# Optimization experiments

Measured on AMD Instinct MI355X. Metric: run time of the kernel, lower is better.

## Reference

```python
import jax, jax.numpy as jnp
import numpy as np
import math

EPS = 1e-8
DIM, HEADS, K = 256, 8, 16
HD = DIM // HEADS
B, N, PDIM = 4, 4096, 3


def _layernorm(x, w, b, eps=1e-5):
    m = jnp.mean(x, axis=-1, keepdims=True)
    v = jnp.mean((x - m) ** 2, axis=-1, keepdims=True)
    return (x - m) * jax.lax.rsqrt(v + eps) * w + b


def setup_inputs() -> dict:
    key = jax.random.key(0)
    ks = jax.random.split(key, 16)
    s = 0.02
    d = {
        'x': jax.random.normal(ks[0], (B, N, DIM), jnp.float32),
        'positions': jax.random.uniform(ks[1], (B, N, PDIM), jnp.float32) * 0.5,  # inside unit ball
        'c': jnp.ones((1,), jnp.float32),
        'time_emb': jax.random.normal(ks[2], (B, DIM), jnp.float32),
        'Wq': jax.random.normal(ks[3], (DIM, DIM), jnp.float32) * s,
        'bq': jnp.zeros((DIM,), jnp.float32),
        'Wk': jax.random.normal(ks[4], (DIM, DIM), jnp.float32) * s,
        'bk': jnp.zeros((DIM,), jnp.float32),
        'Wv': jax.random.normal(ks[5], (DIM, DIM), jnp.float32) * s,
        'bv': jnp.zeros((DIM,), jnp.float32),
        'Wo': jax.random.normal(ks[6], (DIM, DIM), jnp.float32) * s,
        'bo': jnp.zeros((DIM,), jnp.float32),
        'W1': jax.random.normal(ks[7], (DIM, 4 * DIM), jnp.float32) * s,
        'b1': jnp.zeros((4 * DIM,), jnp.float32),
        'W2': jax.random.normal(ks[8], (4 * DIM, DIM), jnp.float32) * s,
        'b2': jnp.zeros((DIM,), jnp.float32),
        'ln1_w': jnp.ones((DIM,), jnp.float32),
        'ln1_b': jnp.zeros((DIM,), jnp.float32),
        'ln2_w': jnp.ones((DIM,), jnp.float32),
        'ln2_b': jnp.zeros((DIM,), jnp.float32),
        'log_tau': jnp.zeros((), jnp.float32),
    }
    return d


def _poincare_dist_matrix(pos, c):
    # pos: [B,N,P], c: scalar > 0. Returns [B,N,N] with d[b,i,j] = dist(pos[b,j], pos[b,i])
    sq = jnp.sum(pos ** 2, axis=-1)                      # [B,N]
    diff2 = (sq[:, :, None] + sq[:, None, :]
             - 2.0 * jnp.einsum('bip,bjp->bij', pos, pos))
    diff2 = jnp.maximum(diff2, 0.0)
    num = 2.0 * c * diff2
    den = (1.0 - c * sq[:, :, None]) * (1.0 - c * sq[:, None, :])
    arg = jnp.maximum(1.0 + num / (den + EPS), 1.0)
    return jnp.arccosh(arg) / jnp.sqrt(c)


def reference(x, positions, c, time_emb, Wq, bq, Wk, bk, Wv, bv, Wo, bo,
              W1, b1, W2, b2, ln1_w, ln1_b, ln2_w, ln2_b, log_tau):
    c_s = jnp.squeeze(c)
    x_res = x
    h = _layernorm(x, ln1_w, ln1_b) + time_emb[:, None, :]

    q = (h @ Wq + bq).reshape(B, N, HEADS, HD).transpose(0, 2, 1, 3)  # [B,H,N,hd]
    k = (h @ Wk + bk).reshape(B, N, HEADS, HD).transpose(0, 2, 1, 3)
    v = (h @ Wv + bv).reshape(B, N, HEADS, HD).transpose(0, 2, 1, 3)

    # pairwise hyperbolic distances + kNN (no_grad in original)
    dist = jax.lax.stop_gradient(_poincare_dist_matrix(positions, c_s))  # [B,N,N]
    neg_vals, idx = jax.lax.top_k(-dist, K)          # smallest-K distances
    attn_dists = -neg_vals                            # [B,N,K]

    # gather neighbor keys/values: out[b,h,n,j,d] = k[b,h,idx[b,n,j],d]
    idx_flat = idx.reshape(B, 1, N * K, 1)            # broadcast over heads, hd
    k_g = jnp.take_along_axis(k, idx_flat, axis=2).reshape(B, HEADS, N, K, HD)
    v_g = jnp.take_along_axis(v, idx_flat, axis=2).reshape(B, HEADS, N, K, HD)

    feat = jnp.einsum('bhnd,bhnkd->bhnk', q, k_g) / math.sqrt(HD)
    tau = jnp.exp(log_tau) + EPS
    scores = feat - attn_dists[:, None, :, :] / tau
    probs = jax.nn.softmax(scores, axis=-1)
    attn = jnp.einsum('bhnk,bhnkd->bhnd', probs, v_g)
    attn = attn.transpose(0, 2, 1, 3).reshape(B, N, DIM)

    x2 = x_res + attn @ Wo + bo
    ff = jax.nn.gelu(_layernorm(x2, ln2_w, ln2_b) @ W1 + b1, approximate=False) @ W2 + b2
    return x2 + ff
```

## Files before the change

### kernel.cpp

```cpp
#include <hip/hip_runtime.h>
#include <math.h>

namespace {

constexpr int kBatch = 4;
constexpr int kN = 4096;
constexpr int kDim = 256;
constexpr int kHeads = 8;
constexpr int kK = 16;
constexpr float kEps = 1e-8f;

using u16 = unsigned short;
typedef __attribute__((ext_vector_type(8))) short short8;
typedef __attribute__((ext_vector_type(8))) u16 u16x8;
typedef __attribute__((ext_vector_type(4))) float f32x4;

__device__ __forceinline__ float b2f(u16 u) {
  union { unsigned int i; float f; } x; x.i = ((unsigned int)u) << 16; return x.f;
}
__device__ __forceinline__ u16 f2b(float f) {
  union { float f; unsigned int i; } x; x.f = f;
  unsigned int r = x.i + 0x7fffu + ((x.i >> 16) & 1u);
  return (u16)(r >> 16);
}
__device__ __forceinline__ float gelu_exact(float x) {
  return 0.5f * x * (1.0f + erff(x * 0.70710678118654752f));
}
__device__ __forceinline__ void load_lds16(const u16* g, u16* l) {
  __builtin_amdgcn_global_load_lds(
      (const __attribute__((address_space(1))) unsigned int*)g,
      (__attribute__((address_space(3))) unsigned int*)l, 16, 0, 0);
}

template<bool ADD_TEMB>
__device__ __forceinline__ void ln_body(
    const float* __restrict__ x, const float* __restrict__ w,
    const float* __restrict__ bb, const float* __restrict__ temb,
    u16* __restrict__ out, int gt) {
  int row = gt >> 6;
  int lane = gt & 63;
  const float4* xr = (const float4*)(x + (size_t)row * kDim);
  float4 v = xr[lane];
  float s = v.x + v.y + v.z + v.w;
  #pragma unroll
  for (int off = 32; off; off >>= 1) s += __shfl_xor(s, off);
  float mean = s * (1.0f / kDim);
  float dx = v.x - mean, dy = v.y - mean, dz = v.z - mean, dw = v.w - mean;
  float ss = dx * dx + dy * dy + dz * dz + dw * dw;
  #pragma unroll
  for (int off = 32; off; off >>= 1) ss += __shfl_xor(ss, off);
  float rstd = rsqrtf(ss * (1.0f / kDim) + 1e-5f);
  float4 wv = ((const float4*)w)[lane];
  float4 bv = ((const float4*)bb)[lane];
  float ox = dx * rstd * wv.x + bv.x;
  float oy = dy * rstd * wv.y + bv.y;
  float oz = dz * rstd * wv.z + bv.z;
  float ow = dw * rstd * wv.w + bv.w;
  if (ADD_TEMB) {
    int bi = row >> 12;
    float4 t = ((const float4*)(temb + (size_t)bi * kDim))[lane];
    ox += t.x; oy += t.y; oz += t.z; ow += t.w;
  }
  ushort4 ob;
  ob.x = f2b(ox); ob.y = f2b(oy); ob.z = f2b(oz); ob.w = f2b(ow);
  ((ushort4*)(out + (size_t)row * kDim))[lane] = ob;
}

__global__ __launch_bounds__(1024, 2) void front_kernel(
    const float* __restrict__ pos, const float* __restrict__ cptr,
    int* __restrict__ idx_out, float* __restrict__ dist_out,
    const float* __restrict__ x, const float* __restrict__ ln1w,
    const float* __restrict__ ln1b, const float* __restrict__ temb,
    u16* __restrict__ h_out,
    const float* __restrict__ Wq, const float* __restrict__ Wk,
    const float* __restrict__ Wv, const float* __restrict__ Wo,
    const float* __restrict__ W1, const float* __restrict__ W2,
    u16* __restrict__ Tq, u16* __restrict__ Tk,
    u16* __restrict__ Tv, u16* __restrict__ To,
    u16* __restrict__ T1, u16* __restrict__ T2) {
  __shared__ float4 ps[kN];
  int tid = threadIdx.x;
  int bx = blockIdx.x;

  if (bx >= 1024) {
    if (bx < 1216) {
      int sub = tid >> 8, stid = tid & 255;
      int task = (bx - 1024) * 4 + sub;
      float* tt = (float*)ps + sub * 1056;
      int seg = task >> 8, e = task & 255;
      const float* W; u16* T; int Kin, Nin, kt, nt;
      if (seg == 0) {
        int which = e >> 6, tl = e & 63;
        W = which == 0 ? Wq : which == 1 ? Wk : which == 2 ? Wv : Wo;
        T = which == 0 ? Tq : which == 1 ? Tk : which == 2 ? Tv : To;
        Kin = 256; Nin = 256; kt = tl >> 3; nt = tl & 7;
      } else if (seg == 1) {
        W = W1; T = T1; Kin = 256; Nin = 1024; kt = e >> 5; nt = e & 31;
      } else {
        W = W2; T = T2; Kin = 1024; Nin = 256; kt = e >> 3; nt = e & 7;
      }
      int tx = stid & 31, ty = stid >> 5;
      #pragma unroll
      for (int rr = 0; rr < 4; ++rr) {
        int r = rr * 8 + ty;
        tt[r * 33 + tx] = W[(size_t)(kt * 32 + r) * Nin + nt * 32 + tx];
      }
      __syncthreads();
      #pragma unroll
      for (int rr = 0; rr < 4; ++rr) {
        int r = rr * 8 + ty;
        T[(size_t)(nt * 32 + r) * Kin + kt * 32 + tx] = f2b(tt[tx * 33 + r]);
      }
    } else {
      ln_body<true>(x, ln1w, ln1b, temb, h_out, (bx - 1216) * 1024 + tid);
    }
    return;
  }

  int wave = tid >> 6, ln = tid & 63;
  int row = bx * 16 + wave;
  int b = row >> 12;
  float c = cptr[0];
  const float* pb = pos + (size_t)b * kN * 3;
  for (int j = tid; j < kN; j += 1024) {
    float px = pb[j * 3 + 0], py = pb[j * 3 + 1], pz = pb[j * 3 + 2];
    ps[j] = make_float4(px, py, pz, c * (px * px + py * py + pz * pz));
  }
  __syncthreads();

  int i = row & (kN - 1);
  float4 pi = ps[i];
  float wi = pi.w, oi = 1.0f - wi;
  float sx = 2.0f * c * pi.x, sy = 2.0f * c * pi.y, sz = 2.0f * c * pi.z;

  auto numden = [&](int j, float& num, float& den) {
    float4 pj = ps[j];
    float tt = wi + pj.w;
    tt = fmaf(-sx, pj.x, tt);
    tt = fmaf(-sy, pj.y, tt);
    tt = fmaf(-sz, pj.z, tt);
    num = fmaxf(tt, 0.0f);
    den = fmaf(-oi, pj.w, oi);
  };
  auto packkey = [&](float num, float den, int j) -> unsigned {
    float r = num * __builtin_amdgcn_rcpf(den);
    union { float f; unsigned u; } cv; cv.f = r;
    return (cv.u & 0xFFFFF000u) | (unsigned)j;
  };
  auto inflate = [&](unsigned T) -> float {
    union { unsigned u; float f; } tv; tv.u = T & 0xFFFFF000u;
    return fmaf(tv.f, 0.001f, tv.f);
  };

  float n0, d0;
  numden(ln, n0, d0);
  unsigned lpk = packkey(n0, d0, ln);
  #pragma unroll
  for (int kk = 2; kk <= 64; kk <<= 1) {
    #pragma unroll
    for (int jj = kk >> 1; jj >= 1; jj >>= 1) {
      unsigned ov = (unsigned)__shfl_xor((int)lpk, jj);
      bool keepMin = (((ln & kk) == 0) == ((ln & jj) == 0));
      bool less = ov < lpk;
      if (keepMin ? less : !less) lpk = ov;
    }
  }
  float Tf = inflate((unsigned)__builtin_amdgcn_readlane((int)lpk, 15));

  auto processGroup = [&](float num, float den, int base) {
    unsigned long long m = __ballot(num < Tf * den);
    if (m) {
      unsigned cpk = packkey(num, den, base + ln);
      do {
        int src = __ffsll(m) - 1;
        m &= m - 1;
        unsigned npk = (unsigned)__builtin_amdgcn_readlane((int)cpk, src);
        unsigned pv = (unsigned)__builtin_amdgcn_update_dpp(
            0, (int)lpk, 0x111 , 0xF, 0xF, false);
        bool gt = lpk > npk;
        bool take = gt && ((ln == 0) || (pv <= npk));
        lpk = take ? npk : (gt ? pv : lpk);
      } while (m);
      Tf = inflate((unsigned)__builtin_amdgcn_readlane((int)lpk, 15));
    }
  };

  int t = 1;
  for (; t + 3 < 64; t += 4) {
    float a0, b0, a1, b1, a2, b2, a3, b3;
    numden(ln + (t + 0) * 64, a0, b0);
    numden(ln + (t + 1) * 64, a1, b1);
    numden(ln + (t + 2) * 64, a2, b2);
    numden(ln + (t + 3) * 64, a3, b3);
    processGroup(a0, b0, (t + 0) * 64);
    processGroup(a1, b1, (t + 1) * 64);
    processGroup(a2, b2, (t + 2) * 64);
    processGroup(a3, b3, (t + 3) * 64);
  }
  for (; t < 64; ++t) {
    float a0, b0;
    numden(ln + t * 64, a0, b0);
    processGroup(a0, b0, t * 64);
  }

  if (ln < kK) {
    int j = (int)(lpk & 0xFFFu);
    float4 pj = ps[j];
    float tt = wi + pj.w;
    tt = fmaf(-sx, pj.x, tt);
    tt = fmaf(-sy, pj.y, tt);
    tt = fmaf(-sz, pj.z, tt);
    float num = 2.0f * fmaxf(tt, 0.0f);
    float den = fmaf(-oi, pj.w, oi) + kEps;
    float arg = fmaxf(1.0f + num / den, 1.0f);
    float rs = 1.0f / sqrtf(c);
    idx_out[(size_t)row * kK + ln] = j;
    dist_out[(size_t)row * kK + ln] = acoshf(arg) * rs;
  }
}

template<int EPI, int BN>
__device__ __forceinline__ void gemm_body(
    const u16* __restrict__ A, const u16* __restrict__ Bt,
    const float* __restrict__ bias, const float* __restrict__ R,
    float* __restrict__ Cf, u16* __restrict__ Cbf,
    int N, int K, int bx, int by) {
  constexpr int NI = BN / 32;
  constexpr int BK = 64;
  __shared__ u16 Al[128 * BK];
  __shared__ u16 Bl[BN * BK];
  int tid = threadIdx.x;
  int wv = tid >> 6, ln = tid & 63;
  int wr = wv >> 1, wc = wv & 1;
  int lhi = ln >> 4, llo = ln & 15;
  int bm = bx * 128, bn = by * BN;

  f32x4 zero = {0.f, 0.f, 0.f, 0.f};
  f32x4 acc[4][NI];
  #pragma unroll
  for (int mi = 0; mi < 4; ++mi)
    #pragma unroll
    for (int ni = 0; ni < NI; ++ni) acc[mi][ni] = zero;

  for (int k0 = 0; k0 < K; k0 += BK) {
    if (k0) __syncthreads();
    #pragma unroll
    for (int i = 0; i < 128 * BK / (8 * 256); ++i) {
      int f = i * 256 + tid;
      int r = f >> 3, o = f & 7;
      load_lds16(A + (size_t)(bm + r) * K + k0 + ((o ^ (r & 7)) << 3),
                 &Al[(i * 256 + wv * 64) * 8]);
    }
    #pragma unroll
    for (int i = 0; i < BN * BK / (8 * 256); ++i) {
      int f = i * 256 + tid;
      int r = f >> 3, o = f & 7;
      load_lds16(Bt + (size_t)(bn + r) * K + k0 + ((o ^ (r & 7)) << 3),
                 &Bl[(i * 256 + wv * 64) * 8]);
    }
    __syncthreads();
    #pragma unroll
    for (int ks = 0; ks < BK; ks += 32) {
      short8 af[4], bf[NI];
      #pragma unroll
      for (int mi = 0; mi < 4; ++mi) {
        int row = wr * 64 + mi * 16 + llo;
        int oct = ((ks >> 3) + lhi) ^ (llo & 7);
        af[mi] = *(const short8*)&Al[row * BK + oct * 8];
      }
      #pragma unroll
      for (int ni = 0; ni < NI; ++ni) {
        int row = wc * (BN / 2) + ni * 16 + llo;
        int oct = ((ks >> 3) + lhi) ^ (llo & 7);
        bf[ni] = *(const short8*)&Bl[row * BK + oct * 8];
      }
      #pragma unroll
      for (int mi = 0; mi < 4; ++mi)
        #pragma unroll
        for (int ni = 0; ni < NI; ++ni)
          acc[mi][ni] = __builtin_amdgcn_mfma_f32_16x16x32_bf16(
              af[mi], bf[ni], acc[mi][ni], 0, 0, 0);
    }
  }

  #pragma unroll
  for (int mi = 0; mi < 4; ++mi) {
    #pragma unroll
    for (int r = 0; r < 4; ++r) {
      int row = bm + wr * 64 + mi * 16 + lhi * 4 + r;
      #pragma unroll
      for (int ni = 0; ni < NI; ++ni) {
        int col = bn + wc * (BN / 2) + ni * 16 + llo;
        float val = acc[mi][ni][r] + bias[col];
        if (EPI == 1) {
          val += R[(size_t)row * N + col];
          Cf[(size_t)row * N + col] = val;
        } else {
          if (EPI == 2) val = gelu_exact(val);
          Cbf[(size_t)row * N + col] = f2b(val);
        }
      }
    }
  }
}

template<int EPI, int BN, int NY>
__global__ __launch_bounds__(256) void gemm_swz_kernel(
    const u16* __restrict__ A, const u16* __restrict__ Bt,
    const float* __restrict__ bias, const float* __restrict__ R,
    float* __restrict__ Cf, u16* __restrict__ Cbf, int N, int K) {
  int cpx = gridDim.x >> 3;
  int orig = blockIdx.x;
  int swz = (orig & 7) * cpx + (orig >> 3);
  int bx = swz / NY, by = swz % NY;
  gemm_body<EPI, BN>(A, Bt, bias, R, Cf, Cbf, N, K, bx, by);
}

__global__ __launch_bounds__(256) void qkv_kernel(
    const u16* __restrict__ A,
    const u16* __restrict__ Bq, const u16* __restrict__ Bk, const u16* __restrict__ Bv,
    const float* __restrict__ bq, const float* __restrict__ bk, const float* __restrict__ bv,
    u16* __restrict__ q, u16* __restrict__ k, u16* __restrict__ v) {
  int cpx = gridDim.x >> 3;
  int orig = blockIdx.x;
  int swz = (orig & 7) * cpx + (orig >> 3);
  int bx = swz / 6, y = swz % 6;
  int sel = y >> 1;
  const u16* Bt = sel == 0 ? Bq : sel == 1 ? Bk : Bv;
  const float* bias = sel == 0 ? bq : sel == 1 ? bk : bv;
  u16* C = sel == 0 ? q : sel == 1 ? k : v;
  gemm_body<0, 128>(A, Bt, bias, nullptr, nullptr, C, 256, 256, bx, y & 1);
}

__global__ __launch_bounds__(512) void wo_ln_kernel(
    const u16* __restrict__ A, const u16* __restrict__ Bt,
    const float* __restrict__ bo, const float* __restrict__ xres,
    const float* __restrict__ ln2w, const float* __restrict__ ln2b,
    float* __restrict__ x2, u16* __restrict__ tln) {
  __shared__ u16 Al[64 * 64];
  __shared__ u16 Bl[256 * 64];
  __shared__ float red[4][64][2];
  int tid = threadIdx.x;
  int wv = tid >> 6, ln = tid & 63;
  int wr = wv >> 2, wc = wv & 3;
  int lhi = ln >> 4, llo = ln & 15;
  int bm = blockIdx.x * 64;

  f32x4 zero = {0.f, 0.f, 0.f, 0.f};
  f32x4 acc[2][4];
  #pragma unroll
  for (int mi = 0; mi < 2; ++mi)
    #pragma unroll
    for (int ni = 0; ni < 4; ++ni) acc[mi][ni] = zero;

  for (int k0 = 0; k0 < 256; k0 += 64) {
    if (k0) __syncthreads();
    {
      int f = tid, r = f >> 3, o = f & 7;
      load_lds16(A + (size_t)(bm + r) * 256 + k0 + ((o ^ (r & 7)) << 3),
                 &Al[(wv * 64) * 8]);
    }
    #pragma unroll
    for (int i = 0; i < 4; ++i) {
      int f = i * 512 + tid, r = f >> 3, o = f & 7;
      load_lds16(Bt + (size_t)r * 256 + k0 + ((o ^ (r & 7)) << 3),
                 &Bl[((i * 8 + wv) * 64) * 8]);
    }
    __syncthreads();
    #pragma unroll
    for (int ks = 0; ks < 64; ks += 32) {
      short8 af[2], bf[4];
      #pragma unroll
      for (int mi = 0; mi < 2; ++mi) {
        int row = wr * 32 + mi * 16 + llo;
        int oct = ((ks >> 3) + lhi) ^ (llo & 7);
        af[mi] = *(const short8*)&Al[row * 64 + oct * 8];
      }
      #pragma unroll
      for (int ni = 0; ni < 4; ++ni) {
        int brow = wc * 64 + ni * 16 + llo;
        int oct = ((ks >> 3) + lhi) ^ (llo & 7);
        bf[ni] = *(const short8*)&Bl[brow * 64 + oct * 8];
      }
      #pragma unroll
      for (int mi = 0; mi < 2; ++mi)
        #pragma unroll
        for (int ni = 0; ni < 4; ++ni)
          acc[mi][ni] = __builtin_amdgcn_mfma_f32_16x16x32_bf16(
              af[mi], bf[ni], acc[mi][ni], 0, 0, 0);
    }
  }

  float psum[2][4], psq[2][4];
  #pragma unroll
  for (int mi = 0; mi < 2; ++mi) {
    #pragma unroll
    for (int r = 0; r < 4; ++r) {
      int row = bm + wr * 32 + mi * 16 + lhi * 4 + r;
      float s = 0.0f, q = 0.0f;
      #pragma unroll
      for (int ni = 0; ni < 4; ++ni) {
        int col = wc * 64 + ni * 16 + llo;
        float v = acc[mi][ni][r] + bo[col] + xres[(size_t)row * 256 + col];
        acc[mi][ni][r] = v;
        s += v;
        q = fmaf(v, v, q);
      }
      #pragma unroll
      for (int off = 1; off < 16; off <<= 1) {
        s += __shfl_xor(s, off);
        q += __shfl_xor(q, off);
      }
      psum[mi][r] = s; psq[mi][r] = q;
    }
  }
  if (llo == 0) {
    #pragma unroll
    for (int mi = 0; mi < 2; ++mi)
      #pragma unroll
      for (int r = 0; r < 4; ++r) {
        int rl = wr * 32 + mi * 16 + lhi * 4 + r;
        red[wc][rl][0] = psum[mi][r];
        red[wc][rl][1] = psq[mi][r];
      }
  }
  __syncthreads();
  constexpr float rn = 1.0f / 256.0f;
  #pragma unroll
  for (int mi = 0; mi < 2; ++mi) {
    #pragma unroll
    for (int r = 0; r < 4; ++r) {
      int rl = wr * 32 + mi * 16 + lhi * 4 + r;
      int row = bm + rl;
      float S = red[0][rl][0] + red[1][rl][0] + red[2][rl][0] + red[3][rl][0];
      float Q = red[0][rl][1] + red[1][rl][1] + red[2][rl][1] + red[3][rl][1];
      float mean = S * rn;
      float var = Q * rn - mean * mean;
      float rstd = rsqrtf(var + 1e-5f);
      #pragma unroll
      for (int ni = 0; ni < 4; ++ni) {
        int col = wc * 64 + ni * 16 + llo;
        float v = acc[mi][ni][r];
        x2[(size_t)row * 256 + col] = v;
        tln[(size_t)row * 256 + col] =
            f2b((v - mean) * rstd * ln2w[col] + ln2b[col]);
      }
    }
  }
}

__global__ __launch_bounds__(256) void attn_kernel(
    const u16* __restrict__ q, const u16* __restrict__ k,
    const u16* __restrict__ v, const int* __restrict__ nidx,
    const float* __restrict__ ndist, const float* __restrict__ log_tau,
    u16* __restrict__ out) {
  int t = blockIdx.x * 256 + threadIdx.x;
  int h = t & (kHeads - 1);
  int row = t >> 3;
  int b = row >> 12;
  float rtau = 1.0f / (expf(log_tau[0]) + kEps);
  const u16x8* qr = (const u16x8*)(q + (size_t)row * kDim + h * 32);
  float qf[32];
  #pragma unroll
  for (int cch = 0; cch < 4; ++cch) {
    u16x8 u = qr[cch];
    #pragma unroll
    for (int e = 0; e < 8; ++e) qf[cch * 8 + e] = b2f(u[e]);
  }

  int njs[kK];
  float sc[kK];
  const int* ir = nidx + (size_t)row * kK;
  const float* dr = ndist + (size_t)row * kK;
  float smax = -1e30f;
  #pragma unroll
  for (int j = 0; j < kK; ++j) {
    int nj = ir[j];
    njs[j] = nj;
    const u16x8* kr = (const u16x8*)(k + ((size_t)b * kN + nj) * kDim + h * 32);
    float dot = 0.0f;
    #pragma unroll
    for (int cch = 0; cch < 4; ++cch) {
      u16x8 u = kr[cch];
      #pragma unroll
      for (int e = 0; e < 8; ++e) dot = fmaf(qf[cch * 8 + e], b2f(u[e]), dot);
    }
    float s = dot * 0.17677669529663687f - dr[j] * rtau;
    sc[j] = s;
    smax = fmaxf(smax, s);
  }
  float sum = 0.0f;
  #pragma unroll
  for (int j = 0; j < kK; ++j) { sc[j] = expf(sc[j] - smax); sum += sc[j]; }
  float rsum = 1.0f / sum;
  float o[32];
  #pragma unroll
  for (int d = 0; d < 32; ++d) o[d] = 0.0f;
  #pragma unroll
  for (int j = 0; j < kK; ++j) {
    float p = sc[j] * rsum;
    const u16x8* vr = (const u16x8*)(v + ((size_t)b * kN + njs[j]) * kDim + h * 32);
    #pragma unroll
    for (int cch = 0; cch < 4; ++cch) {
      u16x8 u = vr[cch];
      #pragma unroll
      for (int e = 0; e < 8; ++e) o[cch * 8 + e] = fmaf(p, b2f(u[e]), o[cch * 8 + e]);
    }
  }
  u16x8* orow = (u16x8*)(out + (size_t)row * kDim + h * 32);
  #pragma unroll
  for (int cch = 0; cch < 4; ++cch) {
    u16x8 po;
    #pragma unroll
    for (int e = 0; e < 8; ++e) po[e] = f2b(o[cch * 8 + e]);
    orow[cch] = po;
  }
}

}

extern "C" void kernel_launch(void* const* d_in, const int* in_sizes, int n_in,
                              void* d_out, int out_size, void* d_ws, size_t ws_size,
                              hipStream_t stream) {
  const float* x    = (const float*)d_in[0];
  const float* pos  = (const float*)d_in[1];
  const float* c    = (const float*)d_in[2];
  const float* temb = (const float*)d_in[3];
  const float* Wq   = (const float*)d_in[4];
  const float* bq   = (const float*)d_in[5];
  const float* Wk   = (const float*)d_in[6];
  const float* bk   = (const float*)d_in[7];
  const float* Wv   = (const float*)d_in[8];
  const float* bv   = (const float*)d_in[9];
  const float* Wo   = (const float*)d_in[10];
  const float* bo   = (const float*)d_in[11];
  const float* W1   = (const float*)d_in[12];
  const float* b1   = (const float*)d_in[13];
  const float* W2   = (const float*)d_in[14];
  const float* b2   = (const float*)d_in[15];
  const float* ln1w = (const float*)d_in[16];
  const float* ln1b = (const float*)d_in[17];
  const float* ln2w = (const float*)d_in[18];
  const float* ln2b = (const float*)d_in[19];
  const float* ltau = (const float*)d_in[20];

  const size_t MB = 1ull << 20;
  char* w = (char*)d_ws;
  u16*   h_bf  = (u16*)(w + 0 * MB);
  u16*   qb    = (u16*)(w + 8 * MB);
  u16*   kb    = (u16*)(w + 16 * MB);
  u16*   vb    = (u16*)(w + 24 * MB);
  u16*   attnb = (u16*)(w + 32 * MB);
  float* x2    = (float*)(w + 40 * MB);
  u16*   g_bf  = (u16*)(w + 56 * MB);
  u16*   wq_t  = (u16*)(w + 88 * MB);
  u16*   wk_t  = wq_t + 65536;
  u16*   wv_t  = wq_t + 2 * 65536;
  u16*   wo_t  = wq_t + 3 * 65536;
  u16*   w1_t  = (u16*)(w + 89 * MB);
  u16*   w2_t  = (u16*)(w + 89 * MB + 512 * 1024);
  int*   kidx  = (int*)(w + 90 * MB);
  float* kdst  = (float*)(w + 91 * MB);
  u16*   tln   = h_bf;

  hipLaunchKernelGGL(front_kernel, dim3(2240), dim3(1024), 0, stream,
                     pos, c, kidx, kdst,
                     x, ln1w, ln1b, temb, h_bf,
                     Wq, Wk, Wv, Wo, W1, W2, wq_t, wk_t, wv_t, wo_t, w1_t, w2_t);
  hipLaunchKernelGGL(qkv_kernel, dim3(768), dim3(256), 0, stream,
                     h_bf, wq_t, wk_t, wv_t, bq, bk, bv, qb, kb, vb);
  hipLaunchKernelGGL(attn_kernel, dim3(512), dim3(256), 0, stream,
                     qb, kb, vb, kidx, kdst, ltau, attnb);
  hipLaunchKernelGGL(wo_ln_kernel, dim3(256), dim3(512), 0, stream,
                     attnb, wo_t, bo, x, ln2w, ln2b, x2, tln);
  hipLaunchKernelGGL((gemm_swz_kernel<2, 128, 8>), dim3(1024), dim3(256), 0, stream,
                     tln, w1_t, b1, nullptr, (float*)nullptr, g_bf, 1024, 256);
  hipLaunchKernelGGL((gemm_swz_kernel<1, 64, 4>), dim3(512), dim3(256), 0, stream,
                     g_bf, w2_t, b2, x2, (float*)d_out, (u16*)nullptr, 256, 1024);
}
```

Measured before the change: 163.2 us.

## Fuse kNN attention into Wo+LayerNorm kernel and simplify kNN threshold test

Removes the standalone attention kernel. Each block of the Wo/LayerNorm kernel now computes the gathered-neighbor attention for its 64 rows and writes the result straight into a swizzled LDS tile, which drops one kernel launch and the global round trip of the attention output. Separately, the kNN scan now does its per-candidate prefilter with a dot product and one FMA compare against precomputed threshold terms, avoiding the num/den work on the hot path. The fused kernel runs only 256 blocks for the gather-heavy attention phase and needs more LDS, so latency hiding for that phase may drop.

```diff
diff --git a/kernel.cpp b/kernel.cpp
--- a/kernel.cpp
+++ b/kernel.cpp
@@ -133,28 +133,30 @@
   float wi = pi.w, oi = 1.0f - wi;
   float sx = 2.0f * c * pi.x, sy = 2.0f * c * pi.y, sz = 2.0f * c * pi.z;
 
-  auto numden = [&](int j, float& num, float& den) {
+  auto dotw = [&](int j, float& S, float& wj) {
     float4 pj = ps[j];
-    float tt = wi + pj.w;
-    tt = fmaf(-sx, pj.x, tt);
-    tt = fmaf(-sy, pj.y, tt);
-    tt = fmaf(-sz, pj.z, tt);
-    num = fmaxf(tt, 0.0f);
-    den = fmaf(-oi, pj.w, oi);
+    S = fmaf(pj.x, sx, fmaf(pj.y, sy, pj.z * sz));
+    wj = pj.w;
   };
-  auto packkey = [&](float num, float den, int j) -> unsigned {
+  auto packkeySW = [&](float S, float wj, int j) -> unsigned {
+    float num = fmaxf(wi + wj - S, 0.0f);
+    float den = fmaf(-oi, wj, oi);
     float r = num * __builtin_amdgcn_rcpf(den);
     union { float f; unsigned u; } cv; cv.f = r;
     return (cv.u & 0xFFFFF000u) | (unsigned)j;
   };
-  auto inflate = [&](unsigned T) -> float {
+
+  float Tf, qq, rhs;
+  auto refresh = [&](unsigned T) {
     union { unsigned u; float f; } tv; tv.u = T & 0xFFFFF000u;
-    return fmaf(tv.f, 0.001f, tv.f);
+    Tf = fmaf(tv.f, 0.001f, tv.f);
+    qq = fmaf(Tf, oi, 1.0f);
+    rhs = fmaf(-Tf, oi, wi);
   };
 
-  float n0, d0;
-  numden(ln, n0, d0);
-  unsigned lpk = packkey(n0, d0, ln);
+  float S0, w0;
+  dotw(ln, S0, w0);
+  unsigned lpk = packkeySW(S0, w0, ln);
   #pragma unroll
   for (int kk = 2; kk <= 64; kk <<= 1) {
     #pragma unroll
@@ -165,12 +167,12 @@
       if (keepMin ? less : !less) lpk = ov;
     }
   }
-  float Tf = inflate((unsigned)__builtin_amdgcn_readlane((int)lpk, 15));
-
-  auto processGroup = [&](float num, float den, int base) {
-    unsigned long long m = __ballot(num < Tf * den);
+  refresh((unsigned)__builtin_amdgcn_readlane((int)lpk, 15));
+
+  auto processGroup = [&](float S, float wj, int base) {
+    unsigned long long m = __ballot(S > fmaf(qq, wj, rhs));
     if (m) {
-      unsigned cpk = packkey(num, den, base + ln);
+      unsigned cpk = packkeySW(S, wj, base + ln);
       do {
         int src = __ffsll(m) - 1;
         m &= m - 1;
@@ -181,26 +183,26 @@
         bool take = gt && ((ln == 0) || (pv <= npk));
         lpk = take ? npk : (gt ? pv : lpk);
       } while (m);
-      Tf = inflate((unsigned)__builtin_amdgcn_readlane((int)lpk, 15));
+      refresh((unsigned)__builtin_amdgcn_readlane((int)lpk, 15));
     }
   };
 
   int t = 1;
   for (; t + 3 < 64; t += 4) {
-    float a0, b0, a1, b1, a2, b2, a3, b3;
-    numden(ln + (t + 0) * 64, a0, b0);
-    numden(ln + (t + 1) * 64, a1, b1);
-    numden(ln + (t + 2) * 64, a2, b2);
-    numden(ln + (t + 3) * 64, a3, b3);
-    processGroup(a0, b0, (t + 0) * 64);
-    processGroup(a1, b1, (t + 1) * 64);
-    processGroup(a2, b2, (t + 2) * 64);
-    processGroup(a3, b3, (t + 3) * 64);
+    float S1, w1, S2, w2, S3, w3, S4, w4;
+    dotw(ln + (t + 0) * 64, S1, w1);
+    dotw(ln + (t + 1) * 64, S2, w2);
+    dotw(ln + (t + 2) * 64, S3, w3);
+    dotw(ln + (t + 3) * 64, S4, w4);
+    processGroup(S1, w1, (t + 0) * 64);
+    processGroup(S2, w2, (t + 1) * 64);
+    processGroup(S3, w3, (t + 2) * 64);
+    processGroup(S4, w4, (t + 3) * 64);
   }
   for (; t < 64; ++t) {
-    float a0, b0;
-    numden(ln + t * 64, a0, b0);
-    processGroup(a0, b0, t * 64);
+    float S1, w1;
+    dotw(ln + t * 64, S1, w1);
+    processGroup(S1, w1, t * 64);
   }
 
   if (ln < kK) {
@@ -332,19 +334,86 @@
   gemm_body<0, 128>(A, Bt, bias, nullptr, nullptr, C, 256, 256, bx, y & 1);
 }
 
-__global__ __launch_bounds__(512) void wo_ln_kernel(
-    const u16* __restrict__ A, const u16* __restrict__ Bt,
-    const float* __restrict__ bo, const float* __restrict__ xres,
+__global__ __launch_bounds__(512) void awo_ln_kernel(
+    const u16* __restrict__ q, const u16* __restrict__ k,
+    const u16* __restrict__ v, const int* __restrict__ nidx,
+    const float* __restrict__ ndist, const float* __restrict__ log_tau,
+    const u16* __restrict__ Bt, const float* __restrict__ bo,
+    const float* __restrict__ xres,
     const float* __restrict__ ln2w, const float* __restrict__ ln2b,
     float* __restrict__ x2, u16* __restrict__ tln) {
-  __shared__ u16 Al[64 * 64];
+  __shared__ u16 Al[64 * 256];
   __shared__ u16 Bl[256 * 64];
   __shared__ float red[4][64][2];
   int tid = threadIdx.x;
+  int bm = blockIdx.x * 64;
+
+  {
+    int rl = tid >> 3, h = tid & 7;
+    int row = bm + rl;
+    int b = row >> 12;
+    float rtau = 1.0f / (expf(log_tau[0]) + kEps);
+    const u16x8* qr = (const u16x8*)(q + (size_t)row * kDim + h * 32);
+    float qf[32];
+    #pragma unroll
+    for (int cch = 0; cch < 4; ++cch) {
+      u16x8 u = qr[cch];
+      #pragma unroll
+      for (int e = 0; e < 8; ++e) qf[cch * 8 + e] = b2f(u[e]);
+    }
+    int njs[kK];
+    float sc[kK];
+    const int* ir = nidx + (size_t)row * kK;
+    const float* dr = ndist + (size_t)row * kK;
+    float smax = -1e30f;
+    #pragma unroll
+    for (int j = 0; j < kK; ++j) {
+      int nj = ir[j];
+      njs[j] = nj;
+      const u16x8* kr = (const u16x8*)(k + ((size_t)b * kN + nj) * kDim + h * 32);
+      float dot = 0.0f;
+      #pragma unroll
+      for (int cch = 0; cch < 4; ++cch) {
+        u16x8 u = kr[cch];
+        #pragma unroll
+        for (int e = 0; e < 8; ++e) dot = fmaf(qf[cch * 8 + e], b2f(u[e]), dot);
+      }
+      float s = dot * 0.17677669529663687f - dr[j] * rtau;
+      sc[j] = s;
+      smax = fmaxf(smax, s);
+    }
+    float sum = 0.0f;
+    #pragma unroll
+    for (int j = 0; j < kK; ++j) { sc[j] = expf(sc[j] - smax); sum += sc[j]; }
+    float rsum = 1.0f / sum;
+    float o[32];
+    #pragma unroll
+    for (int d = 0; d < 32; ++d) o[d] = 0.0f;
+    #pragma unroll
+    for (int j = 0; j < kK; ++j) {
+      float p = sc[j] * rsum;
+      const u16x8* vr = (const u16x8*)(v + ((size_t)b * kN + njs[j]) * kDim + h * 32);
+      #pragma unroll
+      for (int cch = 0; cch < 4; ++cch) {
+        u16x8 u = vr[cch];
+        #pragma unroll
+        for (int e = 0; e < 8; ++e) o[cch * 8 + e] = fmaf(p, b2f(u[e]), o[cch * 8 + e]);
+      }
+    }
+    #pragma unroll
+    for (int cch = 0; cch < 4; ++cch) {
+      u16x8 po;
+      #pragma unroll
+      for (int e = 0; e < 8; ++e) po[e] = f2b(o[cch * 8 + e]);
+      int oct = h * 4 + cch;
+      *(u16x8*)&Al[rl * 256 + ((oct ^ (rl & 7)) << 3)] = po;
+    }
+  }
+  __syncthreads();
+
   int wv = tid >> 6, ln = tid & 63;
   int wr = wv >> 2, wc = wv & 3;
   int lhi = ln >> 4, llo = ln & 15;
-  int bm = blockIdx.x * 64;
 
   f32x4 zero = {0.f, 0.f, 0.f, 0.f};
   f32x4 acc[2][4];
@@ -355,11 +424,6 @@
 
   for (int k0 = 0; k0 < 256; k0 += 64) {
     if (k0) __syncthreads();
-    {
-      int f = tid, r = f >> 3, o = f & 7;
-      load_lds16(A + (size_t)(bm + r) * 256 + k0 + ((o ^ (r & 7)) << 3),
-                 &Al[(wv * 64) * 8]);
-    }
     #pragma unroll
     for (int i = 0; i < 4; ++i) {
       int f = i * 512 + tid, r = f >> 3, o = f & 7;
@@ -373,8 +437,8 @@
       #pragma unroll
       for (int mi = 0; mi < 2; ++mi) {
         int row = wr * 32 + mi * 16 + llo;
-        int oct = ((ks >> 3) + lhi) ^ (llo & 7);
-        af[mi] = *(const short8*)&Al[row * 64 + oct * 8];
+        int octg = ((k0 + ks) >> 3) + lhi;
+        af[mi] = *(const short8*)&Al[row * 256 + ((octg ^ (llo & 7)) << 3)];
       }
       #pragma unroll
       for (int ni = 0; ni < 4; ++ni) {
@@ -397,21 +461,21 @@
     #pragma unroll
     for (int r = 0; r < 4; ++r) {
       int row = bm + wr * 32 + mi * 16 + lhi * 4 + r;
-      float s = 0.0f, q = 0.0f;
+      float s = 0.0f, qv = 0.0f;
       #pragma unroll
       for (int ni = 0; ni < 4; ++ni) {
         int col = wc * 64 + ni * 16 + llo;
-        float v = acc[mi][ni][r] + bo[col] + xres[(size_t)row * 256 + col];
-        acc[mi][ni][r] = v;
-        s += v;
-        q = fmaf(v, v, q);
+        float vv = acc[mi][ni][r] + bo[col] + xres[(size_t)row * 256 + col];
+        acc[mi][ni][r] = vv;
+        s += vv;
+        qv = fmaf(vv, vv, qv);
       }
       #pragma unroll
       for (int off = 1; off < 16; off <<= 1) {
         s += __shfl_xor(s, off);
-        q += __shfl_xor(q, off);
-      }
-      psum[mi][r] = s; psq[mi][r] = q;
+        qv += __shfl_xor(qv, off);
+      }
+      psum[mi][r] = s; psq[mi][r] = qv;
     }
   }
   if (llo == 0) {
@@ -440,80 +504,12 @@
       #pragma unroll
       for (int ni = 0; ni < 4; ++ni) {
         int col = wc * 64 + ni * 16 + llo;
-        float v = acc[mi][ni][r];
-        x2[(size_t)row * 256 + col] = v;
+        float vv = acc[mi][ni][r];
+        x2[(size_t)row * 256 + col] = vv;
         tln[(size_t)row * 256 + col] =
-            f2b((v - mean) * rstd * ln2w[col] + ln2b[col]);
-      }
-    }
-  }
-}
-
-__global__ __launch_bounds__(256) void attn_kernel(
-    const u16* __restrict__ q, const u16* __restrict__ k,
-    const u16* __restrict__ v, const int* __restrict__ nidx,
-    const float* __restrict__ ndist, const float* __restrict__ log_tau,
-    u16* __restrict__ out) {
-  int t = blockIdx.x * 256 + threadIdx.x;
-  int h = t & (kHeads - 1);
-  int row = t >> 3;
-  int b = row >> 12;
-  float rtau = 1.0f / (expf(log_tau[0]) + kEps);
-  const u16x8* qr = (const u16x8*)(q + (size_t)row * kDim + h * 32);
-  float qf[32];
-  #pragma unroll
-  for (int cch = 0; cch < 4; ++cch) {
-    u16x8 u = qr[cch];
-    #pragma unroll
-    for (int e = 0; e < 8; ++e) qf[cch * 8 + e] = b2f(u[e]);
-  }
-
-  int njs[kK];
-  float sc[kK];
-  const int* ir = nidx + (size_t)row * kK;
-  const float* dr = ndist + (size_t)row * kK;
-  float smax = -1e30f;
-  #pragma unroll
-  for (int j = 0; j < kK; ++j) {
-    int nj = ir[j];
-    njs[j] = nj;
-    const u16x8* kr = (const u16x8*)(k + ((size_t)b * kN + nj) * kDim + h * 32);
-    float dot = 0.0f;
-    #pragma unroll
-    for (int cch = 0; cch < 4; ++cch) {
-      u16x8 u = kr[cch];
-      #pragma unroll
-      for (int e = 0; e < 8; ++e) dot = fmaf(qf[cch * 8 + e], b2f(u[e]), dot);
-    }
-    float s = dot * 0.17677669529663687f - dr[j] * rtau;
-    sc[j] = s;
-    smax = fmaxf(smax, s);
-  }
-  float sum = 0.0f;
-  #pragma unroll
-  for (int j = 0; j < kK; ++j) { sc[j] = expf(sc[j] - smax); sum += sc[j]; }
-  float rsum = 1.0f / sum;
-  float o[32];
-  #pragma unroll
-  for (int d = 0; d < 32; ++d) o[d] = 0.0f;
-  #pragma unroll
-  for (int j = 0; j < kK; ++j) {
-    float p = sc[j] * rsum;
-    const u16x8* vr = (const u16x8*)(v + ((size_t)b * kN + njs[j]) * kDim + h * 32);
-    #pragma unroll
-    for (int cch = 0; cch < 4; ++cch) {
-      u16x8 u = vr[cch];
-      #pragma unroll
-      for (int e = 0; e < 8; ++e) o[cch * 8 + e] = fmaf(p, b2f(u[e]), o[cch * 8 + e]);
-    }
-  }
-  u16x8* orow = (u16x8*)(out + (size_t)row * kDim + h * 32);
-  #pragma unroll
-  for (int cch = 0; cch < 4; ++cch) {
-    u16x8 po;
-    #pragma unroll
-    for (int e = 0; e < 8; ++e) po[e] = f2b(o[cch * 8 + e]);
-    orow[cch] = po;
+            f2b((vv - mean) * rstd * ln2w[col] + ln2b[col]);
+      }
+    }
   }
 }
 
@@ -550,7 +546,6 @@
   u16*   qb    = (u16*)(w + 8 * MB);
   u16*   kb    = (u16*)(w + 16 * MB);
   u16*   vb    = (u16*)(w + 24 * MB);
-  u16*   attnb = (u16*)(w + 32 * MB);
   float* x2    = (float*)(w + 40 * MB);
   u16*   g_bf  = (u16*)(w + 56 * MB);
   u16*   wq_t  = (u16*)(w + 88 * MB);
@@ -569,10 +564,9 @@
                      Wq, Wk, Wv, Wo, W1, W2, wq_t, wk_t, wv_t, wo_t, w1_t, w2_t);
   hipLaunchKernelGGL(qkv_kernel, dim3(768), dim3(256), 0, stream,
                      h_bf, wq_t, wk_t, wv_t, bq, bk, bv, qb, kb, vb);
-  hipLaunchKernelGGL(attn_kernel, dim3(512), dim3(256), 0, stream,
-                     qb, kb, vb, kidx, kdst, ltau, attnb);
-  hipLaunchKernelGGL(wo_ln_kernel, dim3(256), dim3(512), 0, stream,
-                     attnb, wo_t, bo, x, ln2w, ln2b, x2, tln);
+  hipLaunchKernelGGL(awo_ln_kernel, dim3(256), dim3(512), 0, stream,
+                     qb, kb, vb, kidx, kdst, ltau,
+                     wo_t, bo, x, ln2w, ln2b, x2, tln);
   hipLaunchKernelGGL((gemm_swz_kernel<2, 128, 8>), dim3(1024), dim3(256), 0, stream,
                      tln, w1_t, b1, nullptr, (float*)nullptr, g_bf, 1024, 256);
   hipLaunchKernelGGL((gemm_swz_kernel<1, 64, 4>), dim3(512), dim3(256), 0, stream,
```

Result: no change. 162.9 us (-0.2%).

## Co-schedule QKV GEMM with kNN blocks and fuse attention into Wo+LN kernel

Applied to the files above, without the earlier changes.

The kNN distance/top-k work moves out of the front kernel into a new mid kernel. Its blocks are interleaved with QKV GEMM blocks so the MFMA-heavy projection overlaps the ALU-heavy distance search. The neighbour attention is fused into the Wo+LayerNorm kernel, which writes attention output straight to LDS in swizzled layout, removing one launch and the attention buffer's round trip through global memory. The cost is that the fused kernel's attention phase runs with only 256 blocks of 512 threads, and the QKV tiles shrink to 128x128 with 1024 threads per block.

```diff
diff --git a/kernel.cpp b/kernel.cpp
--- a/kernel.cpp
+++ b/kernel.cpp
@@ -66,9 +66,7 @@
   ((ushort4*)(out + (size_t)row * kDim))[lane] = ob;
 }
 
-__global__ __launch_bounds__(1024, 2) void front_kernel(
-    const float* __restrict__ pos, const float* __restrict__ cptr,
-    int* __restrict__ idx_out, float* __restrict__ dist_out,
+__global__ __launch_bounds__(1024, 2) void prep_kernel(
     const float* __restrict__ x, const float* __restrict__ ln1w,
     const float* __restrict__ ln1b, const float* __restrict__ temb,
     u16* __restrict__ h_out,
@@ -78,47 +76,126 @@
     u16* __restrict__ Tq, u16* __restrict__ Tk,
     u16* __restrict__ Tv, u16* __restrict__ To,
     u16* __restrict__ T1, u16* __restrict__ T2) {
+  __shared__ float tt4[4][1056];
+  int tid = threadIdx.x;
+  int bx = blockIdx.x;
+  if (bx >= 192) {
+    ln_body<true>(x, ln1w, ln1b, temb, h_out, (bx - 192) * 1024 + tid);
+    return;
+  }
+  int sub = tid >> 8, stid = tid & 255;
+  int task = bx * 4 + sub;
+  float* tt = tt4[sub];
+  int seg = task >> 8, e = task & 255;
+  const float* W; u16* T; int Kin, Nin, kt, nt;
+  if (seg == 0) {
+    int which = e >> 6, tl = e & 63;
+    W = which == 0 ? Wq : which == 1 ? Wk : which == 2 ? Wv : Wo;
+    T = which == 0 ? Tq : which == 1 ? Tk : which == 2 ? Tv : To;
+    Kin = 256; Nin = 256; kt = tl >> 3; nt = tl & 7;
+  } else if (seg == 1) {
+    W = W1; T = T1; Kin = 256; Nin = 1024; kt = e >> 5; nt = e & 31;
+  } else {
+    W = W2; T = T2; Kin = 1024; Nin = 256; kt = e >> 3; nt = e & 7;
+  }
+  int tx = stid & 31, ty = stid >> 5;
+  #pragma unroll
+  for (int rr = 0; rr < 4; ++rr) {
+    int r = rr * 8 + ty;
+    tt[r * 33 + tx] = W[(size_t)(kt * 32 + r) * Nin + nt * 32 + tx];
+  }
+  __syncthreads();
+  #pragma unroll
+  for (int rr = 0; rr < 4; ++rr) {
+    int r = rr * 8 + ty;
+    T[(size_t)(nt * 32 + r) * Kin + kt * 32 + tx] = f2b(tt[tx * 33 + r]);
+  }
+}
+
+__global__ __launch_bounds__(1024, 2) void mid_kernel(
+    const float* __restrict__ pos, const float* __restrict__ cptr,
+    int* __restrict__ idx_out, float* __restrict__ dist_out,
+    const u16* __restrict__ A,
+    const u16* __restrict__ Bq, const u16* __restrict__ Bk, const u16* __restrict__ Bv,
+    const float* __restrict__ bq, const float* __restrict__ bk, const float* __restrict__ bv,
+    u16* __restrict__ qo, u16* __restrict__ ko, u16* __restrict__ vo) {
   __shared__ float4 ps[kN];
   int tid = threadIdx.x;
-  int bx = blockIdx.x;
-
-  if (bx >= 1024) {
-    if (bx < 1216) {
-      int sub = tid >> 8, stid = tid & 255;
-      int task = (bx - 1024) * 4 + sub;
-      float* tt = (float*)ps + sub * 1056;
-      int seg = task >> 8, e = task & 255;
-      const float* W; u16* T; int Kin, Nin, kt, nt;
-      if (seg == 0) {
-        int which = e >> 6, tl = e & 63;
-        W = which == 0 ? Wq : which == 1 ? Wk : which == 2 ? Wv : Wo;
-        T = which == 0 ? Tq : which == 1 ? Tk : which == 2 ? Tv : To;
-        Kin = 256; Nin = 256; kt = tl >> 3; nt = tl & 7;
-      } else if (seg == 1) {
-        W = W1; T = T1; Kin = 256; Nin = 1024; kt = e >> 5; nt = e & 31;
-      } else {
-        W = W2; T = T2; Kin = 1024; Nin = 256; kt = e >> 3; nt = e & 7;
-      }
-      int tx = stid & 31, ty = stid >> 5;
-      #pragma unroll
-      for (int rr = 0; rr < 4; ++rr) {
-        int r = rr * 8 + ty;
-        tt[r * 33 + tx] = W[(size_t)(kt * 32 + r) * Nin + nt * 32 + tx];
+  int bid = blockIdx.x;
+  bool is_qkv = (bid < 1536) && (bid & 1);
+
+  if (is_qkv) {
+    u16* Al = (u16*)ps;
+    u16* Bl = (u16*)ps + 128 * 64;
+    int qid = bid >> 1;
+    int bx = qid / 6, y = qid % 6;
+    int sel = y >> 1, by = y & 1;
+    const u16* Bt = sel == 0 ? Bq : sel == 1 ? Bk : Bv;
+    const float* bias = sel == 0 ? bq : sel == 1 ? bk : bv;
+    u16* C = sel == 0 ? qo : sel == 1 ? ko : vo;
+    int wv = tid >> 6, ln = tid & 63;
+    int wr = wv >> 2, wc = wv & 3;
+    int lhi = ln >> 4, llo = ln & 15;
+    int bm = bx * 128, bn = by * 128;
+
+    f32x4 zero = {0.f, 0.f, 0.f, 0.f};
+    f32x4 acc[2][2];
+    #pragma unroll
+    for (int mi = 0; mi < 2; ++mi)
+      #pragma unroll
+      for (int ni = 0; ni < 2; ++ni) acc[mi][ni] = zero;
+
+    for (int k0 = 0; k0 < 256; k0 += 64) {
+      if (k0) __syncthreads();
+      {
+        int r = tid >> 3, o = tid & 7;
+        load_lds16(A + (size_t)(bm + r) * 256 + k0 + ((o ^ (r & 7)) << 3),
+                   &Al[(wv * 64) * 8]);
+        load_lds16(Bt + (size_t)(bn + r) * 256 + k0 + ((o ^ (r & 7)) << 3),
+                   &Bl[(wv * 64) * 8]);
       }
       __syncthreads();
       #pragma unroll
-      for (int rr = 0; rr < 4; ++rr) {
-        int r = rr * 8 + ty;
-        T[(size_t)(nt * 32 + r) * Kin + kt * 32 + tx] = f2b(tt[tx * 33 + r]);
-      }
-    } else {
-      ln_body<true>(x, ln1w, ln1b, temb, h_out, (bx - 1216) * 1024 + tid);
+      for (int ks = 0; ks < 64; ks += 32) {
+        short8 af[2], bf[2];
+        #pragma unroll
+        for (int mi = 0; mi < 2; ++mi) {
+          int row = wr * 32 + mi * 16 + llo;
+          int oct = ((ks >> 3) + lhi) ^ (llo & 7);
+          af[mi] = *(const short8*)&Al[row * 64 + oct * 8];
+        }
+        #pragma unroll
+        for (int ni = 0; ni < 2; ++ni) {
+          int brow = wc * 32 + ni * 16 + llo;
+          int oct = ((ks >> 3) + lhi) ^ (llo & 7);
+          bf[ni] = *(const short8*)&Bl[brow * 64 + oct * 8];
+        }
+        #pragma unroll
+        for (int mi = 0; mi < 2; ++mi)
+          #pragma unroll
+          for (int ni = 0; ni < 2; ++ni)
+            acc[mi][ni] = __builtin_amdgcn_mfma_f32_16x16x32_bf16(
+                af[mi], bf[ni], acc[mi][ni], 0, 0, 0);
+      }
+    }
+    #pragma unroll
+    for (int mi = 0; mi < 2; ++mi) {
+      #pragma unroll
+      for (int r = 0; r < 4; ++r) {
+        int row = bm + wr * 32 + mi * 16 + lhi * 4 + r;
+        #pragma unroll
+        for (int ni = 0; ni < 2; ++ni) {
+          int col = bn + wc * 32 + ni * 16 + llo;
+          C[(size_t)row * 256 + col] = f2b(acc[mi][ni][r] + bias[col]);
+        }
+      }
     }
     return;
   }
 
+  int tkid = (bid < 1536) ? (bid >> 1) : (bid - 768);
   int wave = tid >> 6, ln = tid & 63;
-  int row = bx * 16 + wave;
+  int row = tkid * 16 + wave;
   int b = row >> 12;
   float c = cptr[0];
   const float* pb = pos + (size_t)b * kN * 3;
@@ -316,35 +393,86 @@
   gemm_body<EPI, BN>(A, Bt, bias, R, Cf, Cbf, N, K, bx, by);
 }
 
-__global__ __launch_bounds__(256) void qkv_kernel(
-    const u16* __restrict__ A,
-    const u16* __restrict__ Bq, const u16* __restrict__ Bk, const u16* __restrict__ Bv,
-    const float* __restrict__ bq, const float* __restrict__ bk, const float* __restrict__ bv,
-    u16* __restrict__ q, u16* __restrict__ k, u16* __restrict__ v) {
-  int cpx = gridDim.x >> 3;
-  int orig = blockIdx.x;
-  int swz = (orig & 7) * cpx + (orig >> 3);
-  int bx = swz / 6, y = swz % 6;
-  int sel = y >> 1;
-  const u16* Bt = sel == 0 ? Bq : sel == 1 ? Bk : Bv;
-  const float* bias = sel == 0 ? bq : sel == 1 ? bk : bv;
-  u16* C = sel == 0 ? q : sel == 1 ? k : v;
-  gemm_body<0, 128>(A, Bt, bias, nullptr, nullptr, C, 256, 256, bx, y & 1);
-}
-
-__global__ __launch_bounds__(512) void wo_ln_kernel(
-    const u16* __restrict__ A, const u16* __restrict__ Bt,
-    const float* __restrict__ bo, const float* __restrict__ xres,
+__global__ __launch_bounds__(512) void awo_ln_kernel(
+    const u16* __restrict__ q, const u16* __restrict__ k,
+    const u16* __restrict__ v, const int* __restrict__ nidx,
+    const float* __restrict__ ndist, const float* __restrict__ log_tau,
+    const u16* __restrict__ Bt, const float* __restrict__ bo,
+    const float* __restrict__ xres,
     const float* __restrict__ ln2w, const float* __restrict__ ln2b,
     float* __restrict__ x2, u16* __restrict__ tln) {
-  __shared__ u16 Al[64 * 64];
+  __shared__ u16 Al[64 * 256];
   __shared__ u16 Bl[256 * 64];
   __shared__ float red[4][64][2];
   int tid = threadIdx.x;
+  int bm = blockIdx.x * 64;
+
+  {
+    int rl = tid >> 3, h = tid & 7;
+    int row = bm + rl;
+    int b = row >> 12;
+    float rtau = 1.0f / (expf(log_tau[0]) + kEps);
+    const u16x8* qr = (const u16x8*)(q + (size_t)row * kDim + h * 32);
+    float qf[32];
+    #pragma unroll
+    for (int cch = 0; cch < 4; ++cch) {
+      u16x8 u = qr[cch];
+      #pragma unroll
+      for (int e = 0; e < 8; ++e) qf[cch * 8 + e] = b2f(u[e]);
+    }
+    int njs[kK];
+    float sc[kK];
+    const int* ir = nidx + (size_t)row * kK;
+    const float* dr = ndist + (size_t)row * kK;
+    float smax = -1e30f;
+    #pragma unroll
+    for (int j = 0; j < kK; ++j) {
+      int nj = ir[j];
+      njs[j] = nj;
+      const u16x8* kr = (const u16x8*)(k + ((size_t)b * kN + nj) * kDim + h * 32);
+      float dot = 0.0f;
+      #pragma unroll
+      for (int cch = 0; cch < 4; ++cch) {
+        u16x8 u = kr[cch];
+        #pragma unroll
+        for (int e = 0; e < 8; ++e) dot = fmaf(qf[cch * 8 + e], b2f(u[e]), dot);
+      }
+      float s = dot * 0.17677669529663687f - dr[j] * rtau;
+      sc[j] = s;
+      smax = fmaxf(smax, s);
+    }
+    float sum = 0.0f;
+    #pragma unroll
+    for (int j = 0; j < kK; ++j) { sc[j] = expf(sc[j] - smax); sum += sc[j]; }
+    float rsum = 1.0f / sum;
+    float o[32];
+    #pragma unroll
+    for (int d = 0; d < 32; ++d) o[d] = 0.0f;
+    #pragma unroll
+    for (int j = 0; j < kK; ++j) {
+      float p = sc[j] * rsum;
+      const u16x8* vr = (const u16x8*)(v + ((size_t)b * kN + njs[j]) * kDim + h * 32);
+      #pragma unroll
+      for (int cch = 0; cch < 4; ++cch) {
+        u16x8 u = vr[cch];
+        #pragma unroll
+        for (int e = 0; e < 8; ++e) o[cch * 8 + e] = fmaf(p, b2f(u[e]), o[cch * 8 + e]);
+      }
+    }
+    #pragma unroll
+    for (int cch = 0; cch < 4; ++cch) {
+      u16x8 po;
+      #pragma unroll
+      for (int e = 0; e < 8; ++e) po[e] = f2b(o[cch * 8 + e]);
+      int oct = h * 4 + cch;
+      *(u16x8*)&Al[rl * 256 + ((oct ^ (rl & 7)) << 3)] = po;
+    }
+  }
+  __syncthreads();
+
   int wv = tid >> 6, ln = tid & 63;
   int wr = wv >> 2, wc = wv & 3;
   int lhi = ln >> 4, llo = ln & 15;
-  int bm = blockIdx.x * 64;
 
   f32x4 zero = {0.f, 0.f, 0.f, 0.f};
   f32x4 acc[2][4];
@@ -355,11 +483,6 @@
 
   for (int k0 = 0; k0 < 256; k0 += 64) {
     if (k0) __syncthreads();
-    {
-      int f = tid, r = f >> 3, o = f & 7;
-      load_lds16(A + (size_t)(bm + r) * 256 + k0 + ((o ^ (r & 7)) << 3),
-                 &Al[(wv * 64) * 8]);
-    }
     #pragma unroll
     for (int i = 0; i < 4; ++i) {
       int f = i * 512 + tid, r = f >> 3, o = f & 7;
@@ -373,8 +496,8 @@
       #pragma unroll
       for (int mi = 0; mi < 2; ++mi) {
         int row = wr * 32 + mi * 16 + llo;
-        int oct = ((ks >> 3) + lhi) ^ (llo & 7);
-        af[mi] = *(const short8*)&Al[row * 64 + oct * 8];
+        int octg = ((k0 + ks) >> 3) + lhi;
+        af[mi] = *(const short8*)&Al[row * 256 + ((octg ^ (llo & 7)) << 3)];
       }
       #pragma unroll
       for (int ni = 0; ni < 4; ++ni) {
@@ -397,21 +520,21 @@
     #pragma unroll
     for (int r = 0; r < 4; ++r) {
       int row = bm + wr * 32 + mi * 16 + lhi * 4 + r;
-      float s = 0.0f, q = 0.0f;
+      float s = 0.0f, qv = 0.0f;
       #pragma unroll
       for (int ni = 0; ni < 4; ++ni) {
         int col = wc * 64 + ni * 16 + llo;
-        float v = acc[mi][ni][r] + bo[col] + xres[(size_t)row * 256 + col];
-        acc[mi][ni][r] = v;
-        s += v;
-        q = fmaf(v, v, q);
+        float vv = acc[mi][ni][r] + bo[col] + xres[(size_t)row * 256 + col];
+        acc[mi][ni][r] = vv;
+        s += vv;
+        qv = fmaf(vv, vv, qv);
       }
       #pragma unroll
       for (int off = 1; off < 16; off <<= 1) {
         s += __shfl_xor(s, off);
-        q += __shfl_xor(q, off);
-      }
-      psum[mi][r] = s; psq[mi][r] = q;
+        qv += __shfl_xor(qv, off);
+      }
+      psum[mi][r] = s; psq[mi][r] = qv;
     }
   }
   if (llo == 0) {
@@ -440,80 +563,12 @@
       #pragma unroll
       for (int ni = 0; ni < 4; ++ni) {
         int col = wc * 64 + ni * 16 + llo;
-        float v = acc[mi][ni][r];
-        x2[(size_t)row * 256 + col] = v;
+        float vv = acc[mi][ni][r];
+        x2[(size_t)row * 256 + col] = vv;
         tln[(size_t)row * 256 + col] =
-            f2b((v - mean) * rstd * ln2w[col] + ln2b[col]);
-      }
-    }
-  }
-}
-
-__global__ __launch_bounds__(256) void attn_kernel(
-    const u16* __restrict__ q, const u16* __restrict__ k,
-    const u16* __restrict__ v, const int* __restrict__ nidx,
-    const float* __restrict__ ndist, const float* __restrict__ log_tau,
-    u16* __restrict__ out) {
-  int t = blockIdx.x * 256 + threadIdx.x;
-  int h = t & (kHeads - 1);
-  int row = t >> 3;
-  int b = row >> 12;
-  float rtau = 1.0f / (expf(log_tau[0]) + kEps);
-  const u16x8* qr = (const u16x8*)(q + (size_t)row * kDim + h * 32);
-  float qf[32];
-  #pragma unroll
-  for (int cch = 0; cch < 4; ++cch) {
-    u16x8 u = qr[cch];
-    #pragma unroll
-    for (int e = 0; e < 8; ++e) qf[cch * 8 + e] = b2f(u[e]);
-  }
-
-  int njs[kK];
-  float sc[kK];
-  const int* ir = nidx + (size_t)row * kK;
-  const float* dr = ndist + (size_t)row * kK;
-  float smax = -1e30f;
-  #pragma unroll
-  for (int j = 0; j < kK; ++j) {
-    int nj = ir[j];
-    njs[j] = nj;
-    const u16x8* kr = (const u16x8*)(k + ((size_t)b * kN + nj) * kDim + h * 32);
-    float dot = 0.0f;
-    #pragma unroll
-    for (int cch = 0; cch < 4; ++cch) {
-      u16x8 u = kr[cch];
-      #pragma unroll
-      for (int e = 0; e < 8; ++e) dot = fmaf(qf[cch * 8 + e], b2f(u[e]), dot);
-    }
-    float s = dot * 0.17677669529663687f - dr[j] * rtau;
-    sc[j] = s;
-    smax = fmaxf(smax, s);
-  }
-  float sum = 0.0f;
-  #pragma unroll
-  for (int j = 0; j < kK; ++j) { sc[j] = expf(sc[j] - smax); sum += sc[j]; }
-  float rsum = 1.0f / sum;
-  float o[32];
-  #pragma unroll
-  for (int d = 0; d < 32; ++d) o[d] = 0.0f;
-  #pragma unroll
-  for (int j = 0; j < kK; ++j) {
-    float p = sc[j] * rsum;
-    const u16x8* vr = (const u16x8*)(v + ((size_t)b * kN + njs[j]) * kDim + h * 32);
-    #pragma unroll
-    for (int cch = 0; cch < 4; ++cch) {
-      u16x8 u = vr[cch];
-      #pragma unroll
-      for (int e = 0; e < 8; ++e) o[cch * 8 + e] = fmaf(p, b2f(u[e]), o[cch * 8 + e]);
-    }
-  }
-  u16x8* orow = (u16x8*)(out + (size_t)row * kDim + h * 32);
-  #pragma unroll
-  for (int cch = 0; cch < 4; ++cch) {
-    u16x8 po;
-    #pragma unroll
-    for (int e = 0; e < 8; ++e) po[e] = f2b(o[cch * 8 + e]);
-    orow[cch] = po;
+            f2b((vv - mean) * rstd * ln2w[col] + ln2b[col]);
+      }
+    }
   }
 }
 
@@ -550,7 +605,6 @@
   u16*   qb    = (u16*)(w + 8 * MB);
   u16*   kb    = (u16*)(w + 16 * MB);
   u16*   vb    = (u16*)(w + 24 * MB);
-  u16*   attnb = (u16*)(w + 32 * MB);
   float* x2    = (float*)(w + 40 * MB);
   u16*   g_bf  = (u16*)(w + 56 * MB);
   u16*   wq_t  = (u16*)(w + 88 * MB);
@@ -563,16 +617,15 @@
   float* kdst  = (float*)(w + 91 * MB);
   u16*   tln   = h_bf;
 
-  hipLaunchKernelGGL(front_kernel, dim3(2240), dim3(1024), 0, stream,
-                     pos, c, kidx, kdst,
+  hipLaunchKernelGGL(prep_kernel, dim3(1216), dim3(1024), 0, stream,
                      x, ln1w, ln1b, temb, h_bf,
                      Wq, Wk, Wv, Wo, W1, W2, wq_t, wk_t, wv_t, wo_t, w1_t, w2_t);
-  hipLaunchKernelGGL(qkv_kernel, dim3(768), dim3(256), 0, stream,
+  hipLaunchKernelGGL(mid_kernel, dim3(1792), dim3(1024), 0, stream,
+                     pos, c, kidx, kdst,
                      h_bf, wq_t, wk_t, wv_t, bq, bk, bv, qb, kb, vb);
-  hipLaunchKernelGGL(attn_kernel, dim3(512), dim3(256), 0, stream,
-                     qb, kb, vb, kidx, kdst, ltau, attnb);
-  hipLaunchKernelGGL(wo_ln_kernel, dim3(256), dim3(512), 0, stream,
-                     attnb, wo_t, bo, x, ln2w, ln2b, x2, tln);
+  hipLaunchKernelGGL(awo_ln_kernel, dim3(256), dim3(512), 0, stream,
+                     qb, kb, vb, kidx, kdst, ltau,
+                     wo_t, bo, x, ln2w, ln2b, x2, tln);
   hipLaunchKernelGGL((gemm_swz_kernel<2, 128, 8>), dim3(1024), dim3(256), 0, stream,
                      tln, w1_t, b1, nullptr, (float*)nullptr, g_bf, 1024, 256);
   hipLaunchKernelGGL((gemm_swz_kernel<1, 64, 4>), dim3(512), dim3(256), 0, stream,
```

After: 176.8 us. +8.3%, slower.
